# Performance work log

Measured on AMD Instinct MI355X. Metric: run time of the kernel, lower is better.

## Reference

```python
import jax, jax.numpy as jnp
import numpy as np

N = 50000
E = 1600000
EP = 500000
D_IN, D_EMB = 64, 32


def setup_inputs() -> dict:
    key = jax.random.key(0)
    ks = jax.random.split(key, 12)
    return {
        "x": jax.random.normal(ks[0], (N, D_IN), dtype=jnp.float32),
        "W1": jax.random.normal(ks[1], (D_IN, D_EMB), dtype=jnp.float32) * (1.0 / np.sqrt(D_IN)),
        "b1": jnp.zeros((D_EMB,), dtype=jnp.float32),
        "W2": jax.random.normal(ks[2], (D_EMB, 2 * D_EMB), dtype=jnp.float32) * (1.0 / np.sqrt(D_EMB)),
        "b2": jnp.zeros((2 * D_EMB,), dtype=jnp.float32),
        "eps": jax.random.normal(ks[3], (N, D_EMB), dtype=jnp.float32),
        "edge_src": jax.random.randint(ks[4], (E,), 0, N, dtype=jnp.int32),
        "edge_dst": jax.random.randint(ks[5], (E,), 0, N, dtype=jnp.int32),
        "pos_src": jax.random.randint(ks[6], (EP,), 0, N, dtype=jnp.int32),
        "pos_dst": jax.random.randint(ks[7], (EP,), 0, N, dtype=jnp.int32),
        "neg_src": jax.random.randint(ks[8], (EP,), 0, N, dtype=jnp.int32),
        "neg_dst": jax.random.randint(ks[9], (EP,), 0, N, dtype=jnp.int32),
    }


def _degree_norms(src, dst, n):
    ones = jnp.ones(src.shape, dtype=jnp.float32)
    out_deg = jax.ops.segment_sum(ones, src, num_segments=n)
    in_deg = jax.ops.segment_sum(ones, dst, num_segments=n)
    # DGL GraphConv norm='both': clamp degrees to >=1, pow(-0.5)
    return jnp.clip(out_deg, 1.0) ** -0.5, jnp.clip(in_deg, 1.0) ** -0.5


def _graph_conv(h, src, dst, norm_src, norm_dst, W, b, n):
    # rst = D_dst^{-1/2} A D_src^{-1/2} h W + b
    msg = (h * norm_src[:, None])[src]                       # [E, d] gather
    agg = jax.ops.segment_sum(msg, dst, num_segments=n)      # [N, d] scatter-add
    return (agg * norm_dst[:, None]) @ W + b


def _dot_predict(z, u, v):
    # u_dot_v: per-edge inner product of endpoint embeddings
    return jnp.sum(z[u] * z[v], axis=-1)


def reference(x, W1, b1, W2, b2, eps, edge_src, edge_dst,
              pos_src, pos_dst, neg_src, neg_dst):
    n = x.shape[0]
    ns, nd = _degree_norms(edge_src, edge_dst, n)
    h = _graph_conv(x, edge_src, edge_dst, ns, nd, W1, b1, n)
    h = jax.nn.relu(h)  # dropout = identity (eval mode)
    h = _graph_conv(h, edge_src, edge_dst, ns, nd, W2, b2, n)
    mu, log_var = jnp.split(h, 2, axis=-1)
    sigma = jnp.exp(log_var / 2.0)
    z = mu + sigma * eps
    pos = _dot_predict(z, pos_src, pos_dst)
    neg = _dot_predict(z, neg_src, neg_dst)
    return pos, neg, mu, sigma
```

## Files before the change

kernel.cpp:

```cpp
#include <hip/hip_runtime.h>
#include <math.h>

#define NN  50000
#define NE  1600000
#define NEP 500000
#define DIN 64
#define DE  32

#define BKT_SH 7
#define NB     391
#define S1B    250
#define CHK    6400
#define HB     128
#define HCHK   12500
#define HWRD   12500
#define XWB    3125

typedef float f4 __attribute__((ext_vector_type(4)));

__device__ __forceinline__ unsigned f2b(float f) {
    unsigned u = __float_as_uint(f);
    return (u + 0x7FFFu + ((u >> 16) & 1u)) >> 16;
}
__device__ __forceinline__ unsigned pack2(float a, float b) {
    return f2b(a) | (f2b(b) << 16);
}
__device__ __forceinline__ float blo(unsigned u) { return __uint_as_float(u << 16); }
__device__ __forceinline__ float bhi(unsigned u) { return __uint_as_float(u & 0xFFFF0000u); }

__global__ __launch_bounds__(256) void k_h1s1(const int* __restrict__ src,
                                              const int* __restrict__ dst,
                                              unsigned* __restrict__ partialS,
                                              unsigned* __restrict__ partialD,
                                              int* __restrict__ T) {
    __shared__ unsigned h[HWRD];
    int t = threadIdx.x;
    if (blockIdx.x < 2 * HB) {
        int isS = blockIdx.x < HB;
        int chunk = isS ? blockIdx.x : blockIdx.x - HB;
        const int* e = isS ? src : dst;
        unsigned* pout = (isS ? partialS : partialD) + (size_t)chunk * HWRD;
        for (int i = t; i < HWRD; i += 256) h[i] = 0;
        __syncthreads();
        int beg = chunk * HCHK;
        const int ev = beg + HCHK;
        int i = beg + t;
        for (; i + 1792 < ev; i += 2048) {
            int s0 = e[i],        s1 = e[i + 256],  s2 = e[i + 512],  s3 = e[i + 768];
            int s4 = e[i + 1024], s5 = e[i + 1280], s6 = e[i + 1536], s7 = e[i + 1792];
            atomicAdd(&h[s0 >> 2], 1u << ((s0 & 3) * 8));
            atomicAdd(&h[s1 >> 2], 1u << ((s1 & 3) * 8));
            atomicAdd(&h[s2 >> 2], 1u << ((s2 & 3) * 8));
            atomicAdd(&h[s3 >> 2], 1u << ((s3 & 3) * 8));
            atomicAdd(&h[s4 >> 2], 1u << ((s4 & 3) * 8));
            atomicAdd(&h[s5 >> 2], 1u << ((s5 & 3) * 8));
            atomicAdd(&h[s6 >> 2], 1u << ((s6 & 3) * 8));
            atomicAdd(&h[s7 >> 2], 1u << ((s7 & 3) * 8));
        }
        for (; i < ev; i += 256) {
            int s = e[i];
            atomicAdd(&h[s >> 2], 1u << ((s & 3) * 8));
        }
        __syncthreads();
        for (int i2 = t; i2 < HWRD; i2 += 256) pout[i2] = h[i2];
    } else {
        int b = blockIdx.x - 2 * HB;
        int* cd = (int*)h;
        for (int i = t; i < NB; i += 256) cd[i] = 0;
        __syncthreads();
        int beg = b * CHK;
        const int ev = beg + CHK;
        int i = beg + t;
        for (; i + 1792 < ev; i += 2048) {
            int d0 = dst[i],        d1 = dst[i + 256],  d2 = dst[i + 512],  d3 = dst[i + 768];
            int d4 = dst[i + 1024], d5 = dst[i + 1280], d6 = dst[i + 1536], d7 = dst[i + 1792];
            atomicAdd(&cd[d0 >> BKT_SH], 1);
            atomicAdd(&cd[d1 >> BKT_SH], 1);
            atomicAdd(&cd[d2 >> BKT_SH], 1);
            atomicAdd(&cd[d3 >> BKT_SH], 1);
            atomicAdd(&cd[d4 >> BKT_SH], 1);
            atomicAdd(&cd[d5 >> BKT_SH], 1);
            atomicAdd(&cd[d6 >> BKT_SH], 1);
            atomicAdd(&cd[d7 >> BKT_SH], 1);
        }
        for (; i < ev; i += 256)
            atomicAdd(&cd[dst[i] >> BKT_SH], 1);
        __syncthreads();
        for (int i2 = t; i2 < NB; i2 += 256) T[b * NB + i2] = cd[i2];
    }
}

__global__ __launch_bounds__(512) void k_s2h(const int* __restrict__ T,
                                             int* __restrict__ Base,
                                             int* __restrict__ BS,
                                             const unsigned* __restrict__ partialS,
                                             const unsigned* __restrict__ partialD,
                                             int* __restrict__ dout,
                                             int* __restrict__ din) {
    int t = threadIdx.x;
    if (blockIdx.x == 0) {
        __shared__ int tot[512];
        int run = 0;
        if (t < NB) {
            for (int b = 0; b < S1B; b += 5) {
                int v0 = T[(b + 0) * NB + t];
                int v1 = T[(b + 1) * NB + t];
                int v2 = T[(b + 2) * NB + t];
                int v3 = T[(b + 3) * NB + t];
                int v4 = T[(b + 4) * NB + t];
                Base[(b + 0) * NB + t] = run; run += v0;
                Base[(b + 1) * NB + t] = run; run += v1;
                Base[(b + 2) * NB + t] = run; run += v2;
                Base[(b + 3) * NB + t] = run; run += v3;
                Base[(b + 4) * NB + t] = run; run += v4;
            }
        }
        tot[t] = (t < NB) ? run : 0;
        __syncthreads();
        for (int off = 1; off < 512; off <<= 1) {
            int v = (t >= off) ? tot[t - off] : 0;
            __syncthreads();
            tot[t] += v;
            __syncthreads();
        }
        if (t < NB) BS[t] = (t == 0) ? 0 : tot[t - 1];
        if (t == 0) BS[NB] = NE;
    } else {
        int half = blockIdx.x >= 26;
        int w = (half ? blockIdx.x - 26 : blockIdx.x - 1) * 512 + t;
        const unsigned* p = half ? partialD : partialS;
        int* dd = half ? din : dout;
        if (w < HWRD) {
            int c0 = 0, c1 = 0, c2 = 0, c3 = 0;
#pragma unroll 8
            for (int b = 0; b < HB; b++) {
                unsigned v = p[(size_t)b * HWRD + w];
                c0 += (int)(v & 0xFFu);
                c1 += (int)((v >> 8) & 0xFFu);
                c2 += (int)((v >> 16) & 0xFFu);
                c3 += (int)(v >> 24);
            }
            ((int4*)dd)[w] = make_int4(c0, c1, c2, c3);
        }
    }
}

__global__ __launch_bounds__(512) void k_s3(const int* __restrict__ src,
                                            const int* __restrict__ dst,
                                            const int* __restrict__ T,
                                            const int* __restrict__ Base,
                                            const int* __restrict__ BS,
                                            unsigned* __restrict__ tmp) {
    __shared__ int scn[512];
    __shared__ int delta[NB];
    __shared__ int cur[NB];
    __shared__ unsigned buf[CHK];
    int t = threadIdx.x;
    int beg = blockIdx.x * CHK;
    scn[t] = (t < NB) ? T[blockIdx.x * NB + t] : 0;
    __syncthreads();
    for (int off = 1; off < 512; off <<= 1) {
        int v = (t >= off) ? scn[t - off] : 0;
        __syncthreads();
        scn[t] += v;
        __syncthreads();
    }
    if (t < NB) {
        int ls = (t == 0) ? 0 : scn[t - 1];
        cur[t] = ls;
        delta[t] = Base[blockIdx.x * NB + t] + BS[t] - ls;
    }
    __syncthreads();
    {
        const int ev = beg + CHK;
        int i = beg + t;
        for (; i + 1536 < ev; i += 2048) {
            int d0 = dst[i],        s0 = src[i];
            int d1 = dst[i + 512],  s1 = src[i + 512];
            int d2 = dst[i + 1024], s2 = src[i + 1024];
            int d3 = dst[i + 1536], s3 = src[i + 1536];
            int l0 = atomicAdd(&cur[d0 >> BKT_SH], 1); buf[l0] = (unsigned)s0 | ((unsigned)d0 << 16);
            int l1 = atomicAdd(&cur[d1 >> BKT_SH], 1); buf[l1] = (unsigned)s1 | ((unsigned)d1 << 16);
            int l2 = atomicAdd(&cur[d2 >> BKT_SH], 1); buf[l2] = (unsigned)s2 | ((unsigned)d2 << 16);
            int l3 = atomicAdd(&cur[d3 >> BKT_SH], 1); buf[l3] = (unsigned)s3 | ((unsigned)d3 << 16);
        }
        for (; i < ev; i += 512) {
            int d = dst[i];
            int s = src[i];
            int lp = atomicAdd(&cur[d >> BKT_SH], 1);
            buf[lp] = (unsigned)s | ((unsigned)d << 16);
        }
    }
    __syncthreads();
    for (int i = t; i < CHK; i += 512) {
        unsigned e = buf[i];
        tmp[delta[e >> (16 + BKT_SH)] + i] = e;
    }
}

__global__ __launch_bounds__(256) void k_s4x(const unsigned* __restrict__ tmp,
                                             const int* __restrict__ BS,
                                             const int* __restrict__ din,
                                             ushort* __restrict__ csr,
                                             int* __restrict__ rowptr,
                                             const float* __restrict__ x,
                                             const float* __restrict__ W1,
                                             const int* __restrict__ dout,
                                             unsigned* __restrict__ xw1b) {
    __shared__ float sW[DIN * DE];
    int t = threadIdx.x;
    if (blockIdx.x < NB) {
        int* scn = (int*)sW;
        int* cur = scn + 128;
        int p = blockIdx.x;
        int ebeg = BS[p];
        int ne = BS[p + 1] - ebeg;
        if (t < 128) {
            int node = (p << BKT_SH) + t;
            scn[t] = (node < NN) ? din[node] : 0;
        }
        __syncthreads();
        for (int off = 1; off < 128; off <<= 1) {
            int v = 0;
            if (t < 128 && t >= off) v = scn[t - off];
            __syncthreads();
            if (t < 128) scn[t] += v;
            __syncthreads();
        }
        if (t < 128) {
            int ex = (t == 0) ? 0 : scn[t - 1];
            cur[t] = ebeg + ex;
            int node = (p << BKT_SH) + t;
            if (node < NN) rowptr[node] = ebeg + ex;
        }
        if (p == NB - 1 && t == 0) rowptr[NN] = NE;
        __syncthreads();
        {
            int i = t;
            for (; i + 768 < ne; i += 1024) {
                unsigned e0 = tmp[ebeg + i];
                unsigned e1 = tmp[ebeg + i + 256];
                unsigned e2 = tmp[ebeg + i + 512];
                unsigned e3 = tmp[ebeg + i + 768];
                int l0 = atomicAdd(&cur[(e0 >> 16) & 127], 1); csr[l0] = (ushort)(e0 & 0xFFFFu);
                int l1 = atomicAdd(&cur[(e1 >> 16) & 127], 1); csr[l1] = (ushort)(e1 & 0xFFFFu);
                int l2 = atomicAdd(&cur[(e2 >> 16) & 127], 1); csr[l2] = (ushort)(e2 & 0xFFFFu);
                int l3 = atomicAdd(&cur[(e3 >> 16) & 127], 1); csr[l3] = (ushort)(e3 & 0xFFFFu);
            }
            for (; i < ne; i += 256) {
                unsigned e = tmp[ebeg + i];
                int lp = atomicAdd(&cur[(e >> 16) & 127], 1);
                csr[lp] = (ushort)(e & 0xFFFFu);
            }
        }
    } else {
        for (int i = t; i < DIN * DE; i += 256) sW[i] = W1[i];
        __syncthreads();
        int r  = (blockIdx.x - NB) * 16 + (t >> 4);
        int tc = t & 15;
        const float* xr = x + (size_t)r * DIN;
        float a0 = 0.f, a1 = 0.f;
#pragma unroll
        for (int k = 0; k < DIN; k++) {
            float v = xr[k];
            a0 += v * sW[k * DE + 2 * tc];
            a1 += v * sW[k * DE + 2 * tc + 1];
        }
        float ns = rsqrtf(fmaxf((float)dout[r], 1.0f));
        xw1b[r * 16 + tc] = pack2(a0 * ns, a1 * ns);
    }
}

__device__ __forceinline__ void acc8(float* a, uint4 w) {
    a[0] += blo(w.x); a[1] += bhi(w.x);
    a[2] += blo(w.y); a[3] += bhi(w.y);
    a[4] += blo(w.z); a[5] += bhi(w.z);
    a[6] += blo(w.w); a[7] += bhi(w.w);
}

__device__ __forceinline__ void gather_row(const ushort* __restrict__ csr,
                                           const uint4* __restrict__ msg,
                                           int beg, int end, int l, float* a) {
    int idx = beg;
    for (; idx + 8 <= end; idx += 8) {
        int s0 = csr[idx],     s1 = csr[idx + 1], s2 = csr[idx + 2], s3 = csr[idx + 3];
        int s4 = csr[idx + 4], s5 = csr[idx + 5], s6 = csr[idx + 6], s7 = csr[idx + 7];
        uint4 w0 = msg[s0 * 4 + l];
        uint4 w1 = msg[s1 * 4 + l];
        uint4 w2 = msg[s2 * 4 + l];
        uint4 w3 = msg[s3 * 4 + l];
        uint4 w4 = msg[s4 * 4 + l];
        uint4 w5 = msg[s5 * 4 + l];
        uint4 w6 = msg[s6 * 4 + l];
        uint4 w7 = msg[s7 * 4 + l];
        acc8(a, w0); acc8(a, w1); acc8(a, w2); acc8(a, w3);
        acc8(a, w4); acc8(a, w5); acc8(a, w6); acc8(a, w7);
    }
    for (; idx + 4 <= end; idx += 4) {
        int s0 = csr[idx], s1 = csr[idx + 1], s2 = csr[idx + 2], s3 = csr[idx + 3];
        uint4 w0 = msg[s0 * 4 + l];
        uint4 w1 = msg[s1 * 4 + l];
        uint4 w2 = msg[s2 * 4 + l];
        uint4 w3 = msg[s3 * 4 + l];
        acc8(a, w0); acc8(a, w1); acc8(a, w2); acc8(a, w3);
    }
    for (; idx < end; idx++) {
        uint4 w = msg[(int)csr[idx] * 4 + l];
        acc8(a, w);
    }
}

__global__ __launch_bounds__(256) void k_g1(const int* __restrict__ rowptr,
                                            const ushort* __restrict__ csr,
                                            const uint4* __restrict__ msg,
                                            const int* __restrict__ dout,
                                            const float* __restrict__ b1,
                                            uint4* __restrict__ out) {
    int t = blockIdx.x * 256 + threadIdx.x;
    int r = t >> 3;
    int l = t & 3;
    int h = (t >> 2) & 1;
    if (r >= NN) return;
    int beg = rowptr[r];
    int end = rowptr[r + 1];
    int mid = beg + ((end - beg) >> 1);
    float a[8] = {0, 0, 0, 0, 0, 0, 0, 0};
    gather_row(csr, msg, h ? mid : beg, h ? end : mid, l, a);
#pragma unroll
    for (int k = 0; k < 8; k++) a[k] += __shfl_xor(a[k], 4);
    if (h) return;
    float scd = rsqrtf(fmaxf((float)(end - beg), 1.0f));
    float scs = rsqrtf(fmaxf((float)dout[r], 1.0f));
    const float4* b14 = (const float4*)b1;
    float4 bb0 = b14[2 * l], bb1 = b14[2 * l + 1];
    float o0 = fmaxf(scd * a[0] + bb0.x, 0.f) * scs;
    float o1 = fmaxf(scd * a[1] + bb0.y, 0.f) * scs;
    float o2 = fmaxf(scd * a[2] + bb0.z, 0.f) * scs;
    float o3 = fmaxf(scd * a[3] + bb0.w, 0.f) * scs;
    float o4 = fmaxf(scd * a[4] + bb1.x, 0.f) * scs;
    float o5 = fmaxf(scd * a[5] + bb1.y, 0.f) * scs;
    float o6 = fmaxf(scd * a[6] + bb1.z, 0.f) * scs;
    float o7 = fmaxf(scd * a[7] + bb1.w, 0.f) * scs;
    out[r * 4 + l] = make_uint4(pack2(o0, o1), pack2(o2, o3), pack2(o4, o5), pack2(o6, o7));
}

__global__ __launch_bounds__(256) void k_g2f(const int* __restrict__ rowptr,
                                             const ushort* __restrict__ csr,
                                             const uint4* __restrict__ msg,
                                             const float* __restrict__ W2,
                                             const float* __restrict__ b2,
                                             const float* __restrict__ eps,
                                             float* __restrict__ mu,
                                             float* __restrict__ sigma,
                                             unsigned* __restrict__ zb) {
    __shared__ float sW[DE * 64];
    __shared__ float sb[64];
    int t = threadIdx.x;
    for (int i = t; i < DE * 64; i += 256) sW[i] = W2[i];
    if (t < 64) sb[t] = b2[t];
    __syncthreads();
    int g = blockIdx.x * 256 + t;
    int r = g >> 3;
    int l = g & 3;
    int j = g & 7;
    int h = (g >> 2) & 1;
    if (r >= NN) return;
    int beg = rowptr[r];
    int end = rowptr[r + 1];
    int mid = beg + ((end - beg) >> 1);
    float a[8] = {0, 0, 0, 0, 0, 0, 0, 0};
    gather_row(csr, msg, h ? mid : beg, h ? end : mid, l, a);
#pragma unroll
    for (int k = 0; k < 8; k++) a[k] += __shfl_xor(a[k], 4);
    float scd = rsqrtf(fmaxf((float)(end - beg), 1.0f));
#pragma unroll
    for (int k = 0; k < 8; k++) a[k] *= scd;
    int cbase = 8 * j;
    float o3[8];
#pragma unroll
    for (int c = 0; c < 8; c++) o3[c] = sb[cbase + c];
#pragma unroll
    for (int d = 0; d < 4; d++) {
        int kb = 8 * (l ^ d);
#pragma unroll
        for (int k = 0; k < 8; k++) {
            float av = (d == 0) ? a[k] : __shfl_xor(a[k], d);
            const float* wrow = sW + (kb + k) * 64 + cbase;
#pragma unroll
            for (int c = 0; c < 8; c++) o3[c] += av * wrow[c];
        }
    }
    if (j < 4) {
        f4* mp = (f4*)(mu + (size_t)r * DE + cbase);
        f4 m0 = {o3[0], o3[1], o3[2], o3[3]};
        f4 m1 = {o3[4], o3[5], o3[6], o3[7]};
        __builtin_nontemporal_store(m0, mp);
        __builtin_nontemporal_store(m1, mp + 1);
    }
    float muv[8];
#pragma unroll
    for (int c = 0; c < 8; c++) muv[c] = __shfl_xor(o3[c], 4);
    if (j >= 4) {
        int cc = cbase - DE;
        const f4* ep = (const f4*)(eps + (size_t)r * DE + cc);
        f4 e0 = __builtin_nontemporal_load(ep);
        f4 e1 = __builtin_nontemporal_load(ep + 1);
        float ev[8] = {e0.x, e0.y, e0.z, e0.w, e1.x, e1.y, e1.z, e1.w};
        float sgv[8], zv[8];
#pragma unroll
        for (int c = 0; c < 8; c++) {
            sgv[c] = expf(0.5f * o3[c]);
            zv[c]  = muv[c] + sgv[c] * ev[c];
        }
        f4* sp = (f4*)(sigma + (size_t)r * DE + cc);
        f4 s0 = {sgv[0], sgv[1], sgv[2], sgv[3]};
        f4 s1 = {sgv[4], sgv[5], sgv[6], sgv[7]};
        __builtin_nontemporal_store(s0, sp);
        __builtin_nontemporal_store(s1, sp + 1);
        uint4* zp = (uint4*)(zb + (size_t)r * 16 + (j - 4) * 4);
        zp[0] = make_uint4(pack2(zv[0], zv[1]), pack2(zv[2], zv[3]),
                           pack2(zv[4], zv[5]), pack2(zv[6], zv[7]));
    }
}

__global__ __launch_bounds__(256) void k_dot2(const uint4* __restrict__ zb4,
                                              const int* __restrict__ pu,
                                              const int* __restrict__ pv,
                                              const int* __restrict__ nu,
                                              const int* __restrict__ nv,
                                              float* __restrict__ out) {
    int t = blockIdx.x * 256 + threadIdx.x;
    int e = t >> 2;
    int l = t & 3;
    if (e < 2 * NEP) {
        int ee = (e < NEP) ? e : e - NEP;
        const int* uu = (e < NEP) ? pu : nu;
        const int* vv = (e < NEP) ? pv : nv;
        int a = __builtin_nontemporal_load(uu + ee);
        int b = __builtin_nontemporal_load(vv + ee);
        uint4 za = zb4[a * 4 + l];
        uint4 zc = zb4[b * 4 + l];
        float s = blo(za.x) * blo(zc.x) + bhi(za.x) * bhi(zc.x)
                + blo(za.y) * blo(zc.y) + bhi(za.y) * bhi(zc.y)
                + blo(za.z) * blo(zc.z) + bhi(za.z) * bhi(zc.z)
                + blo(za.w) * blo(zc.w) + bhi(za.w) * bhi(zc.w);
        s += __shfl_xor(s, 1);
        s += __shfl_xor(s, 2);
        if (l == 0) __builtin_nontemporal_store(s, out + e);
    }
}

extern "C" void kernel_launch(void* const* d_in, const int* in_sizes, int n_in,
                              void* d_out, int out_size, void* d_ws, size_t ws_size,
                              hipStream_t stream) {
    const float* x    = (const float*)d_in[0];
    const float* W1   = (const float*)d_in[1];
    const float* b1   = (const float*)d_in[2];
    const float* W2   = (const float*)d_in[3];
    const float* b2   = (const float*)d_in[4];
    const float* eps  = (const float*)d_in[5];
    const int*   esrc = (const int*)d_in[6];
    const int*   edst = (const int*)d_in[7];
    const int*   psrc = (const int*)d_in[8];
    const int*   pdst = (const int*)d_in[9];
    const int*   gsrc = (const int*)d_in[10];
    const int*   gdst = (const int*)d_in[11];

    float* out = (float*)d_out;
    float* pos = out;
    float* mu  = out + 2 * NEP;
    float* sg  = out + 2 * NEP + NN * DE;

    int* wi = (int*)d_ws;
    int*      rowptr   = wi;
    int*      dout_    = wi + 50004;
    int*      din      = wi + 100004;
    int*      T        = wi + 150004;
    int*      Base     = wi + 247754;
    int*      BS       = wi + 345504;
    ushort*   csr      = (ushort*)(wi + 345896);
    unsigned* partialS = (unsigned*)(wi + 1145896);
    unsigned* partialD = (unsigned*)(wi + 2745896);
    unsigned* tmp      = (unsigned*)(wi + 2745896);
    unsigned* P0       = (unsigned*)(wi + 4345896);
    unsigned* P1       = P0 + 16 * NN;

    k_h1s1<<<2 * HB + S1B, 256, 0, stream>>>(esrc, edst, partialS, partialD, T);
    k_s2h <<<51, 512, 0, stream>>>(T, Base, BS, partialS, partialD, dout_, din);
    k_s3  <<<S1B, 512, 0, stream>>>(esrc, edst, T, Base, BS, tmp);
    k_s4x <<<NB + XWB, 256, 0, stream>>>(tmp, BS, din, csr, rowptr, x, W1, dout_, P0);
    k_g1  <<<(NN * 8 + 255) / 256, 256, 0, stream>>>(rowptr, csr, (const uint4*)P0, dout_, b1, (uint4*)P1);
    k_g2f <<<(NN * 8 + 255) / 256, 256, 0, stream>>>(rowptr, csr, (const uint4*)P1, W2, b2, eps, mu, sg, P0);
    k_dot2<<<(2 * NEP * 4) / 256, 256, 0, stream>>>((const uint4*)P0, psrc, pdst, gsrc, gdst, pos);
}
```

Measured before the change: 200.8 us.

## Pad CSR rows to multiples of eight and fuse dst bucket counts into histogram

Each CSR row is padded to a multiple of 8 entries and filled with a dummy node whose message row is zeroed. Row start and degree are packed into one word per node, so the gather loops read 8 indices at a time with uint4 loads and need no remainder handling. The per-bucket dst counts are now derived from the per-chunk dst histogram, which drops the separate bucket-count pass, and the sort chunking changes to 256 blocks. The cost is more CSR storage and padding work, plus a per-bucket capacity (CAP) that must never overflow and a degree stored in 8 bits.

```diff
diff --git a/kernel.cpp b/kernel.cpp
--- a/kernel.cpp
+++ b/kernel.cpp
@@ -9,12 +9,15 @@
 
 #define BKT_SH 7
 #define NB     391
-#define S1B    250
-#define CHK    6400
-#define HB     128
-#define HCHK   12500
+#define S1B    256
+#define CHK    6250
+#define HBS    128
+#define HCHKS  12500
 #define HWRD   12500
-#define XWB    3125
+#define HWRD2  12512
+#define XWB    3126
+#define CAP    6144
+#define NROW   50016
 
 typedef float f4 __attribute__((ext_vector_type(4)));
 
@@ -28,65 +31,52 @@
 __device__ __forceinline__ float blo(unsigned u) { return __uint_as_float(u << 16); }
 __device__ __forceinline__ float bhi(unsigned u) { return __uint_as_float(u & 0xFFFF0000u); }
 
-__global__ __launch_bounds__(256) void k_h1s1(const int* __restrict__ src,
+__global__ __launch_bounds__(256) void k_hist(const int* __restrict__ src,
                                               const int* __restrict__ dst,
                                               unsigned* __restrict__ partialS,
                                               unsigned* __restrict__ partialD,
                                               int* __restrict__ T) {
-    __shared__ unsigned h[HWRD];
+    __shared__ unsigned h[HWRD2];
     int t = threadIdx.x;
-    if (blockIdx.x < 2 * HB) {
-        int isS = blockIdx.x < HB;
-        int chunk = isS ? blockIdx.x : blockIdx.x - HB;
-        const int* e = isS ? src : dst;
-        unsigned* pout = (isS ? partialS : partialD) + (size_t)chunk * HWRD;
-        for (int i = t; i < HWRD; i += 256) h[i] = 0;
-        __syncthreads();
-        int beg = chunk * HCHK;
-        const int ev = beg + HCHK;
-        int i = beg + t;
-        for (; i + 1792 < ev; i += 2048) {
-            int s0 = e[i],        s1 = e[i + 256],  s2 = e[i + 512],  s3 = e[i + 768];
-            int s4 = e[i + 1024], s5 = e[i + 1280], s6 = e[i + 1536], s7 = e[i + 1792];
-            atomicAdd(&h[s0 >> 2], 1u << ((s0 & 3) * 8));
-            atomicAdd(&h[s1 >> 2], 1u << ((s1 & 3) * 8));
-            atomicAdd(&h[s2 >> 2], 1u << ((s2 & 3) * 8));
-            atomicAdd(&h[s3 >> 2], 1u << ((s3 & 3) * 8));
-            atomicAdd(&h[s4 >> 2], 1u << ((s4 & 3) * 8));
-            atomicAdd(&h[s5 >> 2], 1u << ((s5 & 3) * 8));
-            atomicAdd(&h[s6 >> 2], 1u << ((s6 & 3) * 8));
-            atomicAdd(&h[s7 >> 2], 1u << ((s7 & 3) * 8));
-        }
-        for (; i < ev; i += 256) {
-            int s = e[i];
-            atomicAdd(&h[s >> 2], 1u << ((s & 3) * 8));
-        }
-        __syncthreads();
-        for (int i2 = t; i2 < HWRD; i2 += 256) pout[i2] = h[i2];
-    } else {
-        int b = blockIdx.x - 2 * HB;
-        int* cd = (int*)h;
-        for (int i = t; i < NB; i += 256) cd[i] = 0;
-        __syncthreads();
-        int beg = b * CHK;
-        const int ev = beg + CHK;
-        int i = beg + t;
-        for (; i + 1792 < ev; i += 2048) {
-            int d0 = dst[i],        d1 = dst[i + 256],  d2 = dst[i + 512],  d3 = dst[i + 768];
-            int d4 = dst[i + 1024], d5 = dst[i + 1280], d6 = dst[i + 1536], d7 = dst[i + 1792];
-            atomicAdd(&cd[d0 >> BKT_SH], 1);
-            atomicAdd(&cd[d1 >> BKT_SH], 1);
-            atomicAdd(&cd[d2 >> BKT_SH], 1);
-            atomicAdd(&cd[d3 >> BKT_SH], 1);
-            atomicAdd(&cd[d4 >> BKT_SH], 1);
-            atomicAdd(&cd[d5 >> BKT_SH], 1);
-            atomicAdd(&cd[d6 >> BKT_SH], 1);
-            atomicAdd(&cd[d7 >> BKT_SH], 1);
-        }
-        for (; i < ev; i += 256)
-            atomicAdd(&cd[dst[i] >> BKT_SH], 1);
-        __syncthreads();
-        for (int i2 = t; i2 < NB; i2 += 256) T[b * NB + i2] = cd[i2];
+    int isS = blockIdx.x < HBS;
+    int chunk = isS ? blockIdx.x : blockIdx.x - HBS;
+    const int* e = isS ? src : dst;
+    int chk = isS ? HCHKS : CHK;
+    for (int i = t; i < HWRD2; i += 256) h[i] = 0;
+    __syncthreads();
+    int beg = chunk * chk;
+    const int ev = beg + chk;
+    int i = beg + t;
+    for (; i + 1792 < ev; i += 2048) {
+        int s0 = e[i],        s1 = e[i + 256],  s2 = e[i + 512],  s3 = e[i + 768];
+        int s4 = e[i + 1024], s5 = e[i + 1280], s6 = e[i + 1536], s7 = e[i + 1792];
+        atomicAdd(&h[s0 >> 2], 1u << ((s0 & 3) * 8));
+        atomicAdd(&h[s1 >> 2], 1u << ((s1 & 3) * 8));
+        atomicAdd(&h[s2 >> 2], 1u << ((s2 & 3) * 8));
+        atomicAdd(&h[s3 >> 2], 1u << ((s3 & 3) * 8));
+        atomicAdd(&h[s4 >> 2], 1u << ((s4 & 3) * 8));
+        atomicAdd(&h[s5 >> 2], 1u << ((s5 & 3) * 8));
+        atomicAdd(&h[s6 >> 2], 1u << ((s6 & 3) * 8));
+        atomicAdd(&h[s7 >> 2], 1u << ((s7 & 3) * 8));
+    }
+    for (; i < ev; i += 256) {
+        int s = e[i];
+        atomicAdd(&h[s >> 2], 1u << ((s & 3) * 8));
+    }
+    __syncthreads();
+    unsigned* pout = (isS ? partialS : partialD) + (size_t)chunk * HWRD;
+    for (int i2 = t; i2 < HWRD; i2 += 256) pout[i2] = h[i2];
+    if (!isS) {
+        for (int c = t; c < NB; c += 256) {
+            int sum = 0;
+#pragma unroll
+            for (int k = 0; k < 32; k++) {
+                unsigned v = h[c * 32 + ((k + t) & 31)];
+                sum += (int)(v & 0xFFu) + (int)((v >> 8) & 0xFFu)
+                     + (int)((v >> 16) & 0xFFu) + (int)(v >> 24);
+            }
+            T[chunk * NB + c] = sum;
+        }
     }
 }
 
@@ -102,17 +92,23 @@
         __shared__ int tot[512];
         int run = 0;
         if (t < NB) {
-            for (int b = 0; b < S1B; b += 5) {
+            for (int b = 0; b < S1B; b += 8) {
                 int v0 = T[(b + 0) * NB + t];
                 int v1 = T[(b + 1) * NB + t];
                 int v2 = T[(b + 2) * NB + t];
                 int v3 = T[(b + 3) * NB + t];
                 int v4 = T[(b + 4) * NB + t];
+                int v5 = T[(b + 5) * NB + t];
+                int v6 = T[(b + 6) * NB + t];
+                int v7 = T[(b + 7) * NB + t];
                 Base[(b + 0) * NB + t] = run; run += v0;
                 Base[(b + 1) * NB + t] = run; run += v1;
                 Base[(b + 2) * NB + t] = run; run += v2;
                 Base[(b + 3) * NB + t] = run; run += v3;
                 Base[(b + 4) * NB + t] = run; run += v4;
+                Base[(b + 5) * NB + t] = run; run += v5;
+                Base[(b + 6) * NB + t] = run; run += v6;
+                Base[(b + 7) * NB + t] = run; run += v7;
             }
         }
         tot[t] = (t < NB) ? run : 0;
@@ -125,22 +121,33 @@
         }
         if (t < NB) BS[t] = (t == 0) ? 0 : tot[t - 1];
         if (t == 0) BS[NB] = NE;
-    } else {
-        int half = blockIdx.x >= 26;
-        int w = (half ? blockIdx.x - 26 : blockIdx.x - 1) * 512 + t;
-        const unsigned* p = half ? partialD : partialS;
-        int* dd = half ? din : dout;
+    } else if (blockIdx.x < 26) {
+        int w = (blockIdx.x - 1) * 512 + t;
         if (w < HWRD) {
             int c0 = 0, c1 = 0, c2 = 0, c3 = 0;
 #pragma unroll 8
-            for (int b = 0; b < HB; b++) {
-                unsigned v = p[(size_t)b * HWRD + w];
+            for (int b = 0; b < HBS; b++) {
+                unsigned v = partialS[(size_t)b * HWRD + w];
                 c0 += (int)(v & 0xFFu);
                 c1 += (int)((v >> 8) & 0xFFu);
                 c2 += (int)((v >> 16) & 0xFFu);
                 c3 += (int)(v >> 24);
             }
-            ((int4*)dd)[w] = make_int4(c0, c1, c2, c3);
+            ((int4*)dout)[w] = make_int4(c0, c1, c2, c3);
+        }
+    } else {
+        int w = (blockIdx.x - 26) * 512 + t;
+        if (w < HWRD) {
+            int c0 = 0, c1 = 0, c2 = 0, c3 = 0;
+#pragma unroll 8
+            for (int b = 0; b < S1B; b++) {
+                unsigned v = partialD[(size_t)b * HWRD + w];
+                c0 += (int)(v & 0xFFu);
+                c1 += (int)((v >> 8) & 0xFFu);
+                c2 += (int)((v >> 16) & 0xFFu);
+                c3 += (int)(v >> 24);
+            }
+            ((int4*)din)[w] = make_int4(c0, c1, c2, c3);
         }
     }
 }
@@ -202,7 +209,7 @@
                                              const int* __restrict__ BS,
                                              const int* __restrict__ din,
                                              ushort* __restrict__ csr,
-                                             int* __restrict__ rowptr,
+                                             unsigned* __restrict__ prow,
                                              const float* __restrict__ x,
                                              const float* __restrict__ W1,
                                              const int* __restrict__ dout,
@@ -215,9 +222,11 @@
         int p = blockIdx.x;
         int ebeg = BS[p];
         int ne = BS[p + 1] - ebeg;
+        int myd = 0;
         if (t < 128) {
             int node = (p << BKT_SH) + t;
-            scn[t] = (node < NN) ? din[node] : 0;
+            myd = (node < NN) ? din[node] : 0;
+            scn[t] = (myd + 7) & ~7;
         }
         __syncthreads();
         for (int off = 1; off < 128; off <<= 1) {
@@ -228,12 +237,11 @@
             __syncthreads();
         }
         if (t < 128) {
-            int ex = (t == 0) ? 0 : scn[t - 1];
-            cur[t] = ebeg + ex;
+            int ps = p * CAP + scn[t] - ((myd + 7) & ~7);
+            cur[t] = ps;
             int node = (p << BKT_SH) + t;
-            if (node < NN) rowptr[node] = ebeg + ex;
-        }
-        if (p == NB - 1 && t == 0) rowptr[NN] = NE;
+            if (node < NN) prow[node] = (unsigned)ps | ((unsigned)myd << 24);
+        }
         __syncthreads();
         {
             int i = t;
@@ -253,11 +261,20 @@
                 csr[lp] = (ushort)(e & 0xFFFFu);
             }
         }
+        __syncthreads();
+        if (t < 128) {
+            int end = p * CAP + scn[t];
+            for (int q = cur[t]; q < end; q++) csr[q] = (ushort)NN;
+        }
     } else {
         for (int i = t; i < DIN * DE; i += 256) sW[i] = W1[i];
         __syncthreads();
         int r  = (blockIdx.x - NB) * 16 + (t >> 4);
         int tc = t & 15;
+        if (r >= NN) {
+            if (r < NROW) xw1b[r * 16 + tc] = 0u;
+            return;
+        }
         const float* xr = x + (size_t)r * DIN;
         float a0 = 0.f, a1 = 0.f;
 #pragma unroll
@@ -278,39 +295,35 @@
     a[6] += blo(w.w); a[7] += bhi(w.w);
 }
 
-__device__ __forceinline__ void gather_row(const ushort* __restrict__ csr,
-                                           const uint4* __restrict__ msg,
-                                           int beg, int end, int l, float* a) {
-    int idx = beg;
-    for (; idx + 8 <= end; idx += 8) {
-        int s0 = csr[idx],     s1 = csr[idx + 1], s2 = csr[idx + 2], s3 = csr[idx + 3];
-        int s4 = csr[idx + 4], s5 = csr[idx + 5], s6 = csr[idx + 6], s7 = csr[idx + 7];
-        uint4 w0 = msg[s0 * 4 + l];
-        uint4 w1 = msg[s1 * 4 + l];
-        uint4 w2 = msg[s2 * 4 + l];
-        uint4 w3 = msg[s3 * 4 + l];
-        uint4 w4 = msg[s4 * 4 + l];
-        uint4 w5 = msg[s5 * 4 + l];
-        uint4 w6 = msg[s6 * 4 + l];
-        uint4 w7 = msg[s7 * 4 + l];
-        acc8(a, w0); acc8(a, w1); acc8(a, w2); acc8(a, w3);
-        acc8(a, w4); acc8(a, w5); acc8(a, w6); acc8(a, w7);
-    }
-    for (; idx + 4 <= end; idx += 4) {
-        int s0 = csr[idx], s1 = csr[idx + 1], s2 = csr[idx + 2], s3 = csr[idx + 3];
-        uint4 w0 = msg[s0 * 4 + l];
-        uint4 w1 = msg[s1 * 4 + l];
-        uint4 w2 = msg[s2 * 4 + l];
-        uint4 w3 = msg[s3 * 4 + l];
-        acc8(a, w0); acc8(a, w1); acc8(a, w2); acc8(a, w3);
-    }
-    for (; idx < end; idx++) {
-        uint4 w = msg[(int)csr[idx] * 4 + l];
-        acc8(a, w);
-    }
-}
-
-__global__ __launch_bounds__(256) void k_g1(const int* __restrict__ rowptr,
+__device__ __forceinline__ void gacc(const uint4* __restrict__ msg, uint4 cw, int l, float* a) {
+    uint4 w0 = msg[(int)(cw.x & 0xFFFFu) * 4 + l];
+    uint4 w1 = msg[(int)(cw.x >> 16)     * 4 + l];
+    uint4 w2 = msg[(int)(cw.y & 0xFFFFu) * 4 + l];
+    uint4 w3 = msg[(int)(cw.y >> 16)     * 4 + l];
+    uint4 w4 = msg[(int)(cw.z & 0xFFFFu) * 4 + l];
+    uint4 w5 = msg[(int)(cw.z >> 16)     * 4 + l];
+    uint4 w6 = msg[(int)(cw.w & 0xFFFFu) * 4 + l];
+    uint4 w7 = msg[(int)(cw.w >> 16)     * 4 + l];
+    acc8(a, w0); acc8(a, w1); acc8(a, w2); acc8(a, w3);
+    acc8(a, w4); acc8(a, w5); acc8(a, w6); acc8(a, w7);
+}
+
+__device__ __forceinline__ void gather_half(const ushort* __restrict__ crow,
+                                            const uint4* __restrict__ msg,
+                                            int nb, int h, int l, float* a) {
+    const uint4* cp = (const uint4*)crow;
+    int b = h;
+    if (b >= nb) return;
+    uint4 cur = cp[b];
+    for (b += 2; b < nb; b += 2) {
+        uint4 nxt = cp[b];
+        gacc(msg, cur, l, a);
+        cur = nxt;
+    }
+    gacc(msg, cur, l, a);
+}
+
+__global__ __launch_bounds__(256) void k_g1(const unsigned* __restrict__ prow,
                                             const ushort* __restrict__ csr,
                                             const uint4* __restrict__ msg,
                                             const int* __restrict__ dout,
@@ -320,16 +333,20 @@
     int r = t >> 3;
     int l = t & 3;
     int h = (t >> 2) & 1;
-    if (r >= NN) return;
-    int beg = rowptr[r];
-    int end = rowptr[r + 1];
-    int mid = beg + ((end - beg) >> 1);
+    if (r >= NN) {
+        if (h == 0 && r < NROW) out[r * 4 + l] = make_uint4(0, 0, 0, 0);
+        return;
+    }
+    unsigned pr = prow[r];
+    int ps = (int)(pr & 0xFFFFFFu);
+    int len = (int)(pr >> 24);
+    int nb = (len + 7) >> 3;
     float a[8] = {0, 0, 0, 0, 0, 0, 0, 0};
-    gather_row(csr, msg, h ? mid : beg, h ? end : mid, l, a);
+    gather_half(csr + ps, msg, nb, h, l, a);
 #pragma unroll
     for (int k = 0; k < 8; k++) a[k] += __shfl_xor(a[k], 4);
     if (h) return;
-    float scd = rsqrtf(fmaxf((float)(end - beg), 1.0f));
+    float scd = rsqrtf(fmaxf((float)len, 1.0f));
     float scs = rsqrtf(fmaxf((float)dout[r], 1.0f));
     const float4* b14 = (const float4*)b1;
     float4 bb0 = b14[2 * l], bb1 = b14[2 * l + 1];
@@ -344,7 +361,7 @@
     out[r * 4 + l] = make_uint4(pack2(o0, o1), pack2(o2, o3), pack2(o4, o5), pack2(o6, o7));
 }
 
-__global__ __launch_bounds__(256) void k_g2f(const int* __restrict__ rowptr,
+__global__ __launch_bounds__(256) void k_g2f(const unsigned* __restrict__ prow,
                                              const ushort* __restrict__ csr,
                                              const uint4* __restrict__ msg,
                                              const float* __restrict__ W2,
@@ -365,14 +382,15 @@
     int j = g & 7;
     int h = (g >> 2) & 1;
     if (r >= NN) return;
-    int beg = rowptr[r];
-    int end = rowptr[r + 1];
-    int mid = beg + ((end - beg) >> 1);
+    unsigned pr = prow[r];
+    int ps = (int)(pr & 0xFFFFFFu);
+    int len = (int)(pr >> 24);
+    int nb = (len + 7) >> 3;
     float a[8] = {0, 0, 0, 0, 0, 0, 0, 0};
-    gather_row(csr, msg, h ? mid : beg, h ? end : mid, l, a);
+    gather_half(csr + ps, msg, nb, h, l, a);
 #pragma unroll
     for (int k = 0; k < 8; k++) a[k] += __shfl_xor(a[k], 4);
-    float scd = rsqrtf(fmaxf((float)(end - beg), 1.0f));
+    float scd = rsqrtf(fmaxf((float)len, 1.0f));
 #pragma unroll
     for (int k = 0; k < 8; k++) a[k] *= scd;
     int cbase = 8 * j;
@@ -472,24 +490,24 @@
     float* sg  = out + 2 * NEP + NN * DE;
 
     int* wi = (int*)d_ws;
-    int*      rowptr   = wi;
+    unsigned* prow     = (unsigned*)wi;
     int*      dout_    = wi + 50004;
     int*      din      = wi + 100004;
     int*      T        = wi + 150004;
-    int*      Base     = wi + 247754;
-    int*      BS       = wi + 345504;
-    ushort*   csr      = (ushort*)(wi + 345896);
-    unsigned* partialS = (unsigned*)(wi + 1145896);
-    unsigned* partialD = (unsigned*)(wi + 2745896);
-    unsigned* tmp      = (unsigned*)(wi + 2745896);
-    unsigned* P0       = (unsigned*)(wi + 4345896);
-    unsigned* P1       = P0 + 16 * NN;
-
-    k_h1s1<<<2 * HB + S1B, 256, 0, stream>>>(esrc, edst, partialS, partialD, T);
+    int*      Base     = wi + 250100;
+    int*      BS       = wi + 350196;
+    unsigned* partialS = (unsigned*)(wi + 350592);
+    unsigned* tmp      = partialS;
+    unsigned* partialD = (unsigned*)(wi + 1950592);
+    ushort*   csr      = (ushort*)partialD;
+    unsigned* P0       = (unsigned*)(wi + 5150592);
+    unsigned* P1       = P0 + 16 * NROW;
+
+    k_hist<<<HBS + S1B, 256, 0, stream>>>(esrc, edst, partialS, partialD, T);
     k_s2h <<<51, 512, 0, stream>>>(T, Base, BS, partialS, partialD, dout_, din);
     k_s3  <<<S1B, 512, 0, stream>>>(esrc, edst, T, Base, BS, tmp);
-    k_s4x <<<NB + XWB, 256, 0, stream>>>(tmp, BS, din, csr, rowptr, x, W1, dout_, P0);
-    k_g1  <<<(NN * 8 + 255) / 256, 256, 0, stream>>>(rowptr, csr, (const uint4*)P0, dout_, b1, (uint4*)P1);
-    k_g2f <<<(NN * 8 + 255) / 256, 256, 0, stream>>>(rowptr, csr, (const uint4*)P1, W2, b2, eps, mu, sg, P0);
+    k_s4x <<<NB + XWB, 256, 0, stream>>>(tmp, BS, din, csr, prow, x, W1, dout_, P0);
+    k_g1  <<<(NROW * 8) / 256, 256, 0, stream>>>(prow, csr, (const uint4*)P0, dout_, b1, (uint4*)P1);
+    k_g2f <<<(NN * 8 + 255) / 256, 256, 0, stream>>>(prow, csr, (const uint4*)P1, W2, b2, eps, mu, sg, P0);
     k_dot2<<<(2 * NEP * 4) / 256, 256, 0, stream>>>((const uint4*)P0, psrc, pdst, gsrc, gdst, pos);
 }
```

Measured after the change: 191.9 us. -4.4%, faster.
